# Kernel tuning notes

Hardware: AMD Instinct MI355X
Metric: run time of the kernel (lower is better)

The kernel has to match this reference:

```python
import jax, jax.numpy as jnp
import numpy as np

TEMPERATURE = 0.1
NORMALIZE = True
EPS = 1e-8  # matches torch F.normalize eps-free clamp behavior closely enough for randn inputs

B, D = 4096, 512


def setup_inputs() -> dict:
    key = jax.random.key(0)
    k1, k2 = jax.random.split(key)
    z_i = jax.random.normal(k1, (B, D), dtype=jnp.float32)
    z_j = jax.random.normal(k2, (B, D), dtype=jnp.float32)
    return {"z_i": z_i, "z_j": z_j}


def _l2_normalize(x):
    # torch.F.normalize: x / max(||x||, eps)
    n = jnp.linalg.norm(x, axis=1, keepdims=True)
    return x / jnp.maximum(n, 1e-12)


def reference(z_i, z_j):
    b = z_i.shape[0]
    if NORMALIZE:
        z_i = _l2_normalize(z_i)
        z_j = _l2_normalize(z_j)
    z = jnp.concatenate([z_i, z_j], axis=0)               # (2B, D)
    logits = (z @ z.T) / TEMPERATURE                      # (2B, 2B)
    n = 2 * b
    diag = jnp.eye(n, dtype=bool)
    logits = jnp.where(diag, -jnp.inf, logits)
    row = jnp.arange(n)
    pos_col = (row + b) % n
    pos_logits = logits[row, pos_col]                     # (2B,)
    lse = jax.scipy.special.logsumexp(logits, axis=1)     # stable logsumexp per row
    loss = -(pos_logits - lse).mean()
    return loss
```

## Files before the change

### kernel.cpp

```cpp
#include <hip/hip_runtime.h>
#include <stdint.h>

#define D_DIM 512
#define B_ROWS 4096
#define N_ROWS 8192
#define SCALE_L2E 14.426950408889634f

#define NHP 8
#define NOFF (28 * 256)
#define NBLK (NOFF + 8 * 160)

typedef __attribute__((ext_vector_type(4))) float f32x4;
typedef __attribute__((ext_vector_type(2))) long f8x16;

__global__ __launch_bounds__(256) void k_normalize(const float* __restrict__ zi,
                                                   const float* __restrict__ zj,
                                                   unsigned char* __restrict__ Zn,
                                                   float* __restrict__ pos) {
    const int t = threadIdx.x;
    const int lane = t & 63;
    const int i = blockIdx.x * 4 + (t >> 6);
    const float* pa = zi + (size_t)i * D_DIM + lane * 8;
    const float* pb = zj + (size_t)i * D_DIM + lane * 8;
    const float4 a0 = *(const float4*)pa;
    const float4 a1 = *(const float4*)(pa + 4);
    const float4 b0 = *(const float4*)pb;
    const float4 b1 = *(const float4*)(pb + 4);
    float ssi = a0.x*a0.x + a0.y*a0.y + a0.z*a0.z + a0.w*a0.w
              + a1.x*a1.x + a1.y*a1.y + a1.z*a1.z + a1.w*a1.w;
    float ssj = b0.x*b0.x + b0.y*b0.y + b0.z*b0.z + b0.w*b0.w
              + b1.x*b1.x + b1.y*b1.y + b1.z*b1.z + b1.w*b1.w;
    float dt  = a0.x*b0.x + a0.y*b0.y + a0.z*b0.z + a0.w*b0.w
              + a1.x*b1.x + a1.y*b1.y + a1.z*b1.z + a1.w*b1.w;
    #pragma unroll
    for (int off = 1; off < 64; off <<= 1) {
        ssi += __shfl_xor(ssi, off);
        ssj += __shfl_xor(ssj, off);
        dt  += __shfl_xor(dt,  off);
    }
    const float si = 1.0f / fmaxf(sqrtf(ssi), 1e-12f);
    const float sj = 1.0f / fmaxf(sqrtf(ssj), 1e-12f);
    uint2 pi8, pj8;
    {
        int w0 = 0, w1 = 0;
        w0 = __builtin_amdgcn_cvt_pk_fp8_f32(a0.x * si, a0.y * si, w0, false);
        w0 = __builtin_amdgcn_cvt_pk_fp8_f32(a0.z * si, a0.w * si, w0, true);
        w1 = __builtin_amdgcn_cvt_pk_fp8_f32(a1.x * si, a1.y * si, w1, false);
        w1 = __builtin_amdgcn_cvt_pk_fp8_f32(a1.z * si, a1.w * si, w1, true);
        pi8.x = (unsigned)w0; pi8.y = (unsigned)w1;
        w0 = 0; w1 = 0;
        w0 = __builtin_amdgcn_cvt_pk_fp8_f32(b0.x * sj, b0.y * sj, w0, false);
        w0 = __builtin_amdgcn_cvt_pk_fp8_f32(b0.z * sj, b0.w * sj, w0, true);
        w1 = __builtin_amdgcn_cvt_pk_fp8_f32(b1.x * sj, b1.y * sj, w1, false);
        w1 = __builtin_amdgcn_cvt_pk_fp8_f32(b1.z * sj, b1.w * sj, w1, true);
        pj8.x = (unsigned)w0; pj8.y = (unsigned)w1;
    }
    const size_t PLANE = (size_t)N_ROWS * 64;
    const int o = lane & 7;
    const size_t off0 = (size_t)(lane >> 3) * PLANE + (o & 3) * 16 + (o >> 2) * 8;
    *(uint2*)(Zn + off0 + (size_t)i * 64) = pi8;
    *(uint2*)(Zn + off0 + (size_t)(B_ROWS + i) * 64) = pj8;
    if (lane == 0) pos[i] = 20.0f * dt * si * sj;
}

__global__ __launch_bounds__(64, 3) void k_gemm_lse(const unsigned char* __restrict__ Zn,
                                                    float* __restrict__ rowsum_g) {
    const int lane = threadIdx.x & 63;
    const int l15  = lane & 15, lhi = lane >> 4;

    const int s = (blockIdx.x & 7) * (NBLK / 8) + (blockIdx.x >> 3);
    int SI, SJ, di, dj;
    if (s < NOFF) {
        const int sp = s >> 8;
        int g = s & 255;
        int a = 0, b = 1;
        for (int k = 0; k < sp; ++k) { if (++b == 8) { ++a; b = a + 1; } }
        SI = a; SJ = b;
        const int q = g >> 5, r = g & 31;
        di = r & 15; dj = (r >> 4) * 8 + q;
    } else {
        int g = s - NOFF;
        const int S = g / 160;
        g = g % 160;
        if (g >= 136) return;
        SI = SJ = S;
        di = 0;
        while (g >= 16 - di) { g -= 16 - di; ++di; }
        dj = di + g;
    }
    const int I = SI * 16 + di, J = SJ * 16 + dj;
    const bool dg = (I == J);
    const int rowB = I * 64;
    const int colB = J * 64;

    const char* Zb = (const char*)Zn;
    const size_t PLANE = (size_t)N_ROWS * 64;

    const char* pA = Zb + ((size_t)(rowB + l15)) * 64 + lhi * 16;
    const char* pB = Zb + ((size_t)(colB + l15)) * 64 + lhi * 16;

    f8x16 af0[4], bg0[4], af1[4], bg1[4];

#define LOADAB(dstA, dstB, hp)                                                      \
    do {                                                                            \
        const char* _a = pA + (size_t)(hp) * PLANE;                                 \
        const char* _b = pB + (size_t)(hp) * PLANE;                                 \
        _Pragma("unroll")                                                           \
        for (int mi = 0; mi < 4; ++mi) dstA[mi] = *(const f8x16*)(_a + mi * 1024);  \
        _Pragma("unroll")                                                           \
        for (int ni = 0; ni < 4; ++ni) dstB[ni] = *(const f8x16*)(_b + ni * 1024);  \
    } while (0)

#define MFMAAB(srcA, srcB)                                                          \
    do {                                                                            \
        __builtin_amdgcn_s_setprio(1);                                              \
        _Pragma("unroll")                                                           \
        for (int mi = 0; mi < 4; ++mi)                                              \
            _Pragma("unroll")                                                       \
            for (int ni = 0; ni < 4; ++ni)                                          \
                acc[mi][ni] = __builtin_amdgcn_mfma_f32_16x16x32_fp8_fp8(           \
                    srcA[mi][0], srcB[ni][0], acc[mi][ni], 0, 0, 0);                \
        _Pragma("unroll")                                                           \
        for (int mi = 0; mi < 4; ++mi)                                              \
            _Pragma("unroll")                                                       \
            for (int ni = 0; ni < 4; ++ni)                                          \
                acc[mi][ni] = __builtin_amdgcn_mfma_f32_16x16x32_fp8_fp8(           \
                    srcA[mi][1], srcB[ni][1], acc[mi][ni], 0, 0, 0);                \
        __builtin_amdgcn_s_setprio(0);                                              \
    } while (0)

    f32x4 acc[4][4];
    #pragma unroll
    for (int a = 0; a < 4; ++a)
        #pragma unroll
        for (int b = 0; b < 4; ++b)
            #pragma unroll
            for (int q = 0; q < 4; ++q) acc[a][b][q] = 0.0f;

    LOADAB(af0, bg0, 0);
    #pragma unroll
    for (int hp = 0; hp < NHP; hp += 2) {
        if (hp + 1 < NHP) LOADAB(af1, bg1, hp + 1);
        MFMAAB(af0, bg0);
        if (hp + 2 < NHP) LOADAB(af0, bg0, hp + 2);
        if (hp + 1 < NHP) MFMAAB(af1, bg1);
    }

    float colsum[4] = {0.0f, 0.0f, 0.0f, 0.0f};
    #pragma unroll
    for (int mi = 0; mi < 4; ++mi) {
        const int growb = rowB + mi * 16 + lhi * 4;
        float rs[4] = {0.0f, 0.0f, 0.0f, 0.0f};
        if (dg) {
            #pragma unroll
            for (int ni = 0; ni < 4; ++ni) {
                const int gcol = colB + ni * 16 + l15;
                #pragma unroll
                for (int r = 0; r < 4; ++r) {
                    float arg = acc[mi][ni][r] * SCALE_L2E;
                    if (growb + r == gcol) arg = -1e30f;
                    rs[r] += exp2f(arg);
                }
            }
        } else {
            #pragma unroll
            for (int ni = 0; ni < 4; ++ni)
                #pragma unroll
                for (int r = 0; r < 4; ++r) {
                    const float e = exp2f(acc[mi][ni][r] * SCALE_L2E);
                    rs[r] += e;
                    colsum[ni] += e;
                }
        }
        #pragma unroll
        for (int r = 0; r < 4; ++r) {
            float v = rs[r];
            v += __shfl_xor(v, 1);
            v += __shfl_xor(v, 2);
            v += __shfl_xor(v, 4);
            v += __shfl_xor(v, 8);
            if (l15 == 0) atomicAdd(&rowsum_g[growb + r], v);
        }
    }
    if (!dg) {
        #pragma unroll
        for (int ni = 0; ni < 4; ++ni) {
            float c = colsum[ni];
            c += __shfl_xor(c, 16);
            c += __shfl_xor(c, 32);
            if (lhi == 0)
                atomicAdd(&rowsum_g[colB + ni * 16 + l15], c);
        }
    }
#undef LOADAB
#undef MFMAAB
}

__global__ __launch_bounds__(1024) void k_finalize(const float* __restrict__ rowsum_g,
                                                   const float* __restrict__ pos,
                                                   float* __restrict__ out) {
    const int t = threadIdx.x;
    float l = 0.0f, p = 0.0f;
    #pragma unroll
    for (int q = 0; q < N_ROWS / 1024; ++q) l += logf(rowsum_g[t + q * 1024]);
    #pragma unroll
    for (int q = 0; q < B_ROWS / 1024; ++q) p += pos[t + q * 1024];
    #pragma unroll
    for (int off = 1; off < 64; off <<= 1) {
        l += __shfl_xor(l, off);
        p += __shfl_xor(p, off);
    }
    __shared__ float red[2][16];
    if ((t & 63) == 0) { red[0][t >> 6] = l; red[1][t >> 6] = p; }
    __syncthreads();
    if (t == 0) {
        float L = 0.0f, P = 0.0f;
        #pragma unroll
        for (int q = 0; q < 16; ++q) { L += red[0][q]; P += red[1][q]; }
        out[0] = (L - P) * (1.0f / (float)N_ROWS);
    }
}

extern "C" void kernel_launch(void* const* d_in, const int* in_sizes, int n_in,
                              void* d_out, int out_size, void* d_ws, size_t ws_size,
                              hipStream_t stream) {
    (void)in_sizes; (void)n_in; (void)out_size; (void)ws_size;
    const float* zi = (const float*)d_in[0];
    const float* zj = (const float*)d_in[1];

    const size_t ZN_BYTES = (size_t)N_ROWS * D_DIM;
    unsigned char* Zn     = (unsigned char*)d_ws;
    float* rowsum_g       = (float*)((char*)d_ws + ZN_BYTES);
    float* pos            = (float*)((char*)d_ws + ZN_BYTES + N_ROWS * 4);

    hipMemsetAsync(rowsum_g, 0, N_ROWS * 4, stream);

    k_normalize<<<B_ROWS / 4, 256, 0, stream>>>(zi, zj, Zn, pos);
    k_gemm_lse<<<NBLK, 64, 0, stream>>>(Zn, rowsum_g);
    k_finalize<<<1, 1024, 0, stream>>>(rowsum_g, pos, (float*)d_out);
}
```

Measured before the change: 57.58 us.

## Widen GEMM tile to 64x128 per wave and fold rowsum zeroing into normalize

Each single-wave block of the symmetric GEMM+LSE kernel now computes a 64x128 tile instead of 64x64, remapping the upper-triangle tile schedule into 128x128 cells split into row halves, with per-half masking on diagonal cells. This raises MFMA work per A-fragment load and halves the number of blocks and atomic row/column-sum traffic per output. In exchange it doubles the accumulator and B-fragment register footprint, so occupancy is reduced from 3 to 2 waves per SIMD. The separate memset of the row sums is removed and done by the first blocks of the normalize kernel, saving a launch.

```diff
diff --git a/kernel.cpp b/kernel.cpp
--- a/kernel.cpp
+++ b/kernel.cpp
@@ -7,8 +7,11 @@
 #define SCALE_L2E 14.426950408889634f
 
 #define NHP 8
-#define NOFF (28 * 256)
-#define NBLK (NOFF + 8 * 160)
+#define NOFFS (28 * 128)
+#define NBLK (NOFFS + 8 * 72)
+#define WM_NONE 0
+#define WM_DIAG 1
+#define WM_FULL 2
 
 typedef __attribute__((ext_vector_type(4))) float f32x4;
 typedef __attribute__((ext_vector_type(2))) long f8x16;
@@ -16,8 +19,13 @@
 __global__ __launch_bounds__(256) void k_normalize(const float* __restrict__ zi,
                                                    const float* __restrict__ zj,
                                                    unsigned char* __restrict__ Zn,
-                                                   float* __restrict__ pos) {
+                                                   float* __restrict__ pos,
+                                                   float* __restrict__ rowsum_g) {
     const int t = threadIdx.x;
+    if (blockIdx.x < 8) {
+        float4 z = {0.0f, 0.0f, 0.0f, 0.0f};
+        *(float4*)(rowsum_g + blockIdx.x * 1024 + t * 4) = z;
+    }
     const int lane = t & 63;
     const int i = blockIdx.x * 4 + (t >> 6);
     const float* pa = zi + (size_t)i * D_DIM + lane * 8;
@@ -63,35 +71,40 @@
     if (lane == 0) pos[i] = 20.0f * dt * si * sj;
 }
 
-__global__ __launch_bounds__(64, 3) void k_gemm_lse(const unsigned char* __restrict__ Zn,
+__global__ __launch_bounds__(64, 2) void k_gemm_lse(const unsigned char* __restrict__ Zn,
                                                     float* __restrict__ rowsum_g) {
     const int lane = threadIdx.x & 63;
     const int l15  = lane & 15, lhi = lane >> 4;
 
     const int s = (blockIdx.x & 7) * (NBLK / 8) + (blockIdx.x >> 3);
-    int SI, SJ, di, dj;
-    if (s < NOFF) {
-        const int sp = s >> 8;
-        int g = s & 255;
-        int a = 0, b = 1;
-        for (int k = 0; k < sp; ++k) { if (++b == 8) { ++a; b = a + 1; } }
-        SI = a; SJ = b;
-        const int q = g >> 5, r = g & 31;
-        di = r & 15; dj = (r >> 4) * 8 + q;
+    int a, b, half;
+    if (s < NOFFS) {
+        const int sp = s >> 7;
+        const int u  = s & 127;
+        int A0 = 0, B0 = 1;
+        for (int k = 0; k < sp; ++k) { if (++B0 == 8) { ++A0; B0 = A0 + 1; } }
+        const int cell = u >> 1;
+        a = A0 * 8 + (cell >> 3);
+        b = B0 * 8 + (cell & 7);
+        half = u & 1;
     } else {
-        int g = s - NOFF;
-        const int S = g / 160;
-        g = g % 160;
-        if (g >= 136) return;
-        SI = SJ = S;
-        di = 0;
-        while (g >= 16 - di) { g -= 16 - di; ++di; }
-        dj = di + g;
-    }
-    const int I = SI * 16 + di, J = SJ * 16 + dj;
-    const bool dg = (I == J);
-    const int rowB = I * 64;
-    const int colB = J * 64;
+        int v = s - NOFFS;
+        const int S = v / 72; v %= 72;
+        const int c = v >> 1;
+        half = v & 1;
+        int di = 0, g = c;
+        while (g >= 8 - di) { g -= 8 - di; ++di; }
+        a = S * 8 + di;
+        b = S * 8 + di + g;
+    }
+    const bool dgcell = (a == b);
+    int m0 = WM_FULL, m1 = WM_FULL;
+    if (dgcell) {
+        if (half == 0) { m0 = WM_DIAG; m1 = WM_FULL; }
+        else           { m0 = WM_NONE; m1 = WM_DIAG; }
+    }
+    const int rowB = (2 * a + half) * 64;
+    const int colB = 2 * b * 64;
 
     const char* Zb = (const char*)Zn;
     const size_t PLANE = (size_t)N_ROWS * 64;
@@ -99,7 +112,7 @@
     const char* pA = Zb + ((size_t)(rowB + l15)) * 64 + lhi * 16;
     const char* pB = Zb + ((size_t)(colB + l15)) * 64 + lhi * 16;
 
-    f8x16 af0[4], bg0[4], af1[4], bg1[4];
+    f8x16 af0[4], af1[4], bg0[8], bg1[8];
 
 #define LOADAB(dstA, dstB, hp)                                                      \
     do {                                                                            \
@@ -108,7 +121,7 @@
         _Pragma("unroll")                                                           \
         for (int mi = 0; mi < 4; ++mi) dstA[mi] = *(const f8x16*)(_a + mi * 1024);  \
         _Pragma("unroll")                                                           \
-        for (int ni = 0; ni < 4; ++ni) dstB[ni] = *(const f8x16*)(_b + ni * 1024);  \
+        for (int ni = 0; ni < 8; ++ni) dstB[ni] = *(const f8x16*)(_b + ni * 1024);  \
     } while (0)
 
 #define MFMAAB(srcA, srcB)                                                          \
@@ -117,25 +130,25 @@
         _Pragma("unroll")                                                           \
         for (int mi = 0; mi < 4; ++mi)                                              \
             _Pragma("unroll")                                                       \
-            for (int ni = 0; ni < 4; ++ni)                                          \
+            for (int ni = 0; ni < 8; ++ni)                                          \
                 acc[mi][ni] = __builtin_amdgcn_mfma_f32_16x16x32_fp8_fp8(           \
                     srcA[mi][0], srcB[ni][0], acc[mi][ni], 0, 0, 0);                \
         _Pragma("unroll")                                                           \
         for (int mi = 0; mi < 4; ++mi)                                              \
             _Pragma("unroll")                                                       \
-            for (int ni = 0; ni < 4; ++ni)                                          \
+            for (int ni = 0; ni < 8; ++ni)                                          \
                 acc[mi][ni] = __builtin_amdgcn_mfma_f32_16x16x32_fp8_fp8(           \
                     srcA[mi][1], srcB[ni][1], acc[mi][ni], 0, 0, 0);                \
         __builtin_amdgcn_s_setprio(0);                                              \
     } while (0)
 
-    f32x4 acc[4][4];
-    #pragma unroll
-    for (int a = 0; a < 4; ++a)
-        #pragma unroll
-        for (int b = 0; b < 4; ++b)
-            #pragma unroll
-            for (int q = 0; q < 4; ++q) acc[a][b][q] = 0.0f;
+    f32x4 acc[4][8];
+    #pragma unroll
+    for (int x = 0; x < 4; ++x)
+        #pragma unroll
+        for (int y = 0; y < 8; ++y)
+            #pragma unroll
+            for (int q = 0; q < 4; ++q) acc[x][y][q] = 0.0f;
 
     LOADAB(af0, bg0, 0);
     #pragma unroll
@@ -146,12 +159,21 @@
         if (hp + 1 < NHP) MFMAAB(af1, bg1);
     }
 
-    float colsum[4] = {0.0f, 0.0f, 0.0f, 0.0f};
+    float colsum[8] = {0.0f, 0.0f, 0.0f, 0.0f, 0.0f, 0.0f, 0.0f, 0.0f};
     #pragma unroll
     for (int mi = 0; mi < 4; ++mi) {
         const int growb = rowB + mi * 16 + lhi * 4;
         float rs[4] = {0.0f, 0.0f, 0.0f, 0.0f};
-        if (dg) {
+        if (m0 == WM_FULL) {
+            #pragma unroll
+            for (int ni = 0; ni < 4; ++ni)
+                #pragma unroll
+                for (int r = 0; r < 4; ++r) {
+                    const float e = exp2f(acc[mi][ni][r] * SCALE_L2E);
+                    rs[r] += e;
+                    colsum[ni] += e;
+                }
+        } else if (m0 == WM_DIAG) {
             #pragma unroll
             for (int ni = 0; ni < 4; ++ni) {
                 const int gcol = colB + ni * 16 + l15;
@@ -162,15 +184,27 @@
                     rs[r] += exp2f(arg);
                 }
             }
-        } else {
-            #pragma unroll
-            for (int ni = 0; ni < 4; ++ni)
+        }
+        if (m1 == WM_FULL) {
+            #pragma unroll
+            for (int ni = 4; ni < 8; ++ni)
                 #pragma unroll
                 for (int r = 0; r < 4; ++r) {
                     const float e = exp2f(acc[mi][ni][r] * SCALE_L2E);
                     rs[r] += e;
                     colsum[ni] += e;
                 }
+        } else {
+            #pragma unroll
+            for (int ni = 4; ni < 8; ++ni) {
+                const int gcol = colB + ni * 16 + l15;
+                #pragma unroll
+                for (int r = 0; r < 4; ++r) {
+                    float arg = acc[mi][ni][r] * SCALE_L2E;
+                    if (growb + r == gcol) arg = -1e30f;
+                    rs[r] += exp2f(arg);
+                }
+            }
         }
         #pragma unroll
         for (int r = 0; r < 4; ++r) {
@@ -182,14 +216,22 @@
             if (l15 == 0) atomicAdd(&rowsum_g[growb + r], v);
         }
     }
-    if (!dg) {
+    if (m0 == WM_FULL) {
         #pragma unroll
         for (int ni = 0; ni < 4; ++ni) {
             float c = colsum[ni];
             c += __shfl_xor(c, 16);
             c += __shfl_xor(c, 32);
-            if (lhi == 0)
-                atomicAdd(&rowsum_g[colB + ni * 16 + l15], c);
+            if (lhi == 0) atomicAdd(&rowsum_g[colB + ni * 16 + l15], c);
+        }
+    }
+    if (m1 == WM_FULL) {
+        #pragma unroll
+        for (int ni = 4; ni < 8; ++ni) {
+            float c = colsum[ni];
+            c += __shfl_xor(c, 16);
+            c += __shfl_xor(c, 32);
+            if (lhi == 0) atomicAdd(&rowsum_g[colB + ni * 16 + l15], c);
         }
     }
 #undef LOADAB
@@ -233,9 +275,7 @@
     float* rowsum_g       = (float*)((char*)d_ws + ZN_BYTES);
     float* pos            = (float*)((char*)d_ws + ZN_BYTES + N_ROWS * 4);
 
-    hipMemsetAsync(rowsum_g, 0, N_ROWS * 4, stream);
-
-    k_normalize<<<B_ROWS / 4, 256, 0, stream>>>(zi, zj, Zn, pos);
+    k_normalize<<<B_ROWS / 4, 256, 0, stream>>>(zi, zj, Zn, pos, rowsum_g);
     k_gemm_lse<<<NBLK, 64, 0, stream>>>(Zn, rowsum_g);
     k_finalize<<<1, 1024, 0, stream>>>(rowsum_g, pos, (float*)d_out);
 }
```

New measurement: 56.09 us. -2.6%, faster.
